# Optimization experiments

Measured on AMD Instinct MI355X. Metric: run time of the kernel, lower is better.

Reference implementation:

```python
import jax, jax.numpy as jnp
import numpy as np

R_MAX = 6.0
NUM_BASIS = 8
TANH_N = 6.0
RECYCLES = 3
N_NODES = 20000
N_EDGES = 640000
ATTR_DIM = 64
LATENT = 64
LN_EPS = 1e-5


def _layer_norm(x, g, b):
    m = x.mean(-1, keepdims=True)
    v = x.var(-1, keepdims=True)
    return (x - m) * jax.lax.rsqrt(v + LN_EPS) * g + b


def setup_inputs() -> dict:
    key = jax.random.key(0)
    ks = jax.random.split(key, 16)
    d1 = 2 * ATTR_DIM + NUM_BASIS  # 136, edge_feature_mlp input
    d2 = LATENT + ATTR_DIM         # 128, attn_mlp input
    d3 = 2 * LATENT                # 128, latent_update_mlp input
    s1 = 1.0 / np.sqrt(d1)
    s2 = 1.0 / np.sqrt(d2)
    s3 = 1.0 / np.sqrt(d3)
    sf = 1.0 / np.sqrt(NUM_BASIS)
    sg = 1.0 / np.sqrt(2 * LATENT)
    return {
        "edge_index": jax.random.randint(ks[0], (2, N_EDGES), 0, N_NODES, dtype=jnp.int64),
        "edge_length": jax.random.uniform(ks[1], (N_EDGES,), minval=0.5, maxval=R_MAX, dtype=jnp.float32),
        "node_attrs": jax.random.normal(ks[2], (N_NODES, ATTR_DIM), dtype=jnp.float32),
        "ln1_g": jnp.ones((d1,), jnp.float32), "ln1_b": jnp.zeros((d1,), jnp.float32),
        "W1": jax.random.normal(ks[3], (d1, LATENT), jnp.float32) * s1,
        "b1": jnp.zeros((LATENT,), jnp.float32),
        "ln2_g": jnp.ones((d2,), jnp.float32), "ln2_b": jnp.zeros((d2,), jnp.float32),
        "W2": jax.random.normal(ks[4], (d2, 1), jnp.float32) * s2,
        "b2": jnp.zeros((1,), jnp.float32),
        "ln3_g": jnp.ones((d3,), jnp.float32), "ln3_b": jnp.zeros((d3,), jnp.float32),
        "W3": jax.random.normal(ks[5], (d3, LATENT), jnp.float32) * s3,
        "b3": jnp.zeros((LATENT,), jnp.float32),
        "film_W1": jax.random.normal(ks[6], (NUM_BASIS, 4 * LATENT), jnp.float32) * sf,  # swiglu: 2*(2*latent)
        "film_W2": jax.random.normal(ks[7], (2 * LATENT, LATENT), jnp.float32) * sg,
        "resnet_p": jnp.zeros((1,), jnp.float32),
    }


def reference(edge_index, edge_length, node_attrs,
              ln1_g, ln1_b, W1, b1,
              ln2_g, ln2_b, W2, b2,
              ln3_g, ln3_b, W3, b3,
              film_W1, film_W2, resnet_p):
    ec = edge_index[0]
    en = edge_index[1]
    num_nodes = node_attrs.shape[0]
    num_edges = edge_index.shape[1]

    # Bessel radial basis * tanh cutoff
    n = jnp.arange(1, NUM_BASIS + 1, dtype=jnp.float32)
    r = edge_length[:, None]
    bessel = jnp.sqrt(2.0 / R_MAX) * jnp.sin(n * jnp.pi * r / R_MAX) / r  # [E, B]
    cutoff = jnp.tanh(1.0 - (edge_length / R_MAX) ** TANH_N) ** 3          # [E]
    rbf = bessel * cutoff[:, None]                                         # [E, B]

    a_c = node_attrs[ec]  # [E, A] gathered center attrs
    a_n = node_attrs[en]  # [E, A] gathered neighbor attrs

    latents = jnp.zeros((num_edges, LATENT), dtype=jnp.float32)
    for _ in range(RECYCLES):  # num_layers=1, recycles=3 -> 3 block applications
        edge_in = jnp.concatenate([a_c, a_n, rbf], axis=-1)            # [E, 136]
        ef = _layer_norm(edge_in, ln1_g, ln1_b) @ W1 + b1              # [E, L]
        attn_in = jnp.concatenate([ef, a_c], axis=-1)                  # [E, 128]
        scores = (_layer_norm(attn_in, ln2_g, ln2_b) @ W2 + b2)[:, 0]  # [E]
        attn = jax.nn.softmax(scores, axis=0)                          # global edge softmax
        pooled = jax.ops.segment_sum(attn[:, None] * ef, ec, num_segments=num_nodes)  # [N, L]
        upd_in = jnp.concatenate([ef, pooled[ec]], axis=-1)            # [E, 2L]
        upd = _layer_norm(upd_in, ln3_g, ln3_b) @ W3 + b3              # [E, L]
        # FiLM gate from rbf: swiglu hidden then sigmoid output, no bias
        h = rbf @ film_W1                                              # [E, 4L]
        a, g = jnp.split(h, 2, axis=-1)
        gate = jax.nn.sigmoid((jax.nn.silu(a) * g) @ film_W2)          # [E, L]
        upd = upd * gate
        uc = jax.nn.sigmoid(resnet_p)                                  # [1]
        c_old = jax.lax.rsqrt(uc * uc + 1.0)
        latents = c_old * latents + (uc * c_old) * upd
    return latents
```

## Files before the change

kernel.cpp:

```cpp
#include <hip/hip_runtime.h>
#include <math.h>

#define KNOTS 1024
#define LNE 1e-5f
#define R0F 0.5f
#define RMAXF 6.0f
#define PAD 96

__device__ __forceinline__ float hermite_(float v0, float m0, float v1, float m1, float t){
  float A = v1 - v0;
  return v0 + t*(m0 + t*((3.f*A - 2.f*m0 - m1) + t*(m0 + m1 - 2.f*A)));
}

__device__ __forceinline__ float wsum64(float v){
#pragma unroll
  for(int m=32;m>=1;m>>=1) v += __shfl_xor(v, m, 64);
  return v;
}

__global__ __launch_bounds__(256) void k_zero(int* cnt, float* sumExp, int N){
  int i = blockIdx.x*256 + threadIdx.x;
  if(i < N) cnt[i] = 0;
  if(i == 0) sumExp[0] = 0.f;
}

__global__ __launch_bounds__(256) void k_weights(
    const float* ln1_g, const float* ln1_b, const float* W1, const float* b1,
    const float* ln2_g, const float* ln2_b, const float* W2, const float* b2,
    const float* ln3_g, const float* ln3_b, const float* W3, const float* b3,
    const float* resnet_p,
    float* W1gA, float* W1gB, float* W1gBot, float* W3gTop, float* W3gBot,
    float* colsum1, float* c1, float* colsum3, float* c3, float* W2g,
    float* cs1w3, float* c1w3, float* BW3, float* misc){
  int tid = threadIdx.x;
  for(int idx=tid; idx<4096; idx+=256){
    int k = idx>>6;
    W1gA[idx]   = ln1_g[k]*W1[idx];
    W1gB[idx]   = ln1_g[64+k]*W1[4096+idx];
    W3gTop[idx] = ln3_g[k]*W3[idx];
    W3gBot[idx] = ln3_g[64+k]*W3[4096+idx];
  }
  for(int idx=tid; idx<512; idx+=256) W1gBot[idx] = ln1_g[128+(idx>>6)]*W1[8192+idx];
  if(tid<128) W2g[tid] = ln2_g[tid]*W2[tid];
  if(tid<64){
    float cs=0.f, cc=0.f;
    for(int k=0;k<136;k++){ float wv = W1[k*64+tid]; cs += ln1_g[k]*wv; cc += ln1_b[k]*wv; }
    colsum1[tid] = cs; c1[tid] = cc + b1[tid];
    float cs3=0.f, cc3=0.f;
    for(int k=0;k<128;k++){ float wv = W3[k*64+tid]; cs3 += ln3_g[k]*wv; cc3 += ln3_b[k]*wv; }
    colsum3[tid] = cs3; c3[tid] = cc3 + b3[tid];
  }
  if(tid==0){
    float cs2=0.f, cc2=0.f;
    for(int k=0;k<128;k++){ cs2 += ln2_g[k]*W2[k]; cc2 += ln2_b[k]*W2[k]; }
    misc[0]=cs2; misc[1]=cc2 + b2[0];
    float p = resnet_p[0];
    float uc = 1.f/(1.f+expf(-p));
    float co = rsqrtf(uc*uc+1.f);
    misc[2] = uc*co*(1.f + co + co*co);
  }
  __syncthreads();
  if(tid<64){
    float a=0.f, b=0.f;
    for(int k=0;k<64;k++){ float wv = W3gTop[k*64+tid]; a += colsum1[k]*wv; b += c1[k]*wv; }
    cs1w3[tid]=a; c1w3[tid]=b;
  }
  for(int idx=tid; idx<512; idx+=256){
    int kk = idx>>6, j = idx&63;
    float a=0.f;
    for(int k=0;k<64;k++) a += W1gBot[kk*64+k]*W3gTop[k*64+j];
    BW3[idx]=a;
  }
  if(tid==0){
    float a=0.f,b=0.f;
    for(int k=0;k<64;k++){ a += colsum1[k]*W2g[k]; b += c1[k]*W2g[k]; }
    misc[3]=a; misc[4]=b;
    float a5=0.f, a6=0.f;
    for(int k=0;k<64;k++){ a5 += colsum1[k]; a6 += c1[k]; }
    misc[5]=a5; misc[6]=a6;
  }
  if(tid<8){
    float a=0.f;
    for(int k=0;k<64;k++) a += W1gBot[tid*64+k]*W2g[k];
    misc[8+tid]=a;
  }
}

__device__ __forceinline__ void eval_all(
    float r, const float* W1gBot, const float* BW3, const float* bw2,
    const float* F1, const float* F2, float* uL, int lane,
    float& T1, float& T13, float& T12, float& gate, float& sr, float& sq){
  float rbf[8];
  float inv_r = 1.f/r;
  float x = r*(1.f/6.f);
  float x2 = x*x;
  float x6 = x2*x2*x2;
  float th = tanhf(1.f - x6);
  float cut = th*th*th;
  float pref = 0.57735026919f*inv_r*cut;
  sr=0.f; sq=0.f;
#pragma unroll
  for(int n=0;n<8;n++){
    float b = pref*sinf((float)(n+1)*0.52359877559f*r);
    rbf[n]=b; sr+=b; sq+=b*b;
  }
  float t1=0.f,t3=0.f,t2=0.f;
#pragma unroll
  for(int k=0;k<8;k++){
    t1 += rbf[k]*W1gBot[k*64+lane];
    t3 += rbf[k]*BW3[k*64+lane];
    t2 += rbf[k]*bw2[k];
  }
  T1=t1; T13=t3; T12=t2;
  float a0=0.f,a1=0.f,g0=0.f,g1=0.f;
#pragma unroll
  for(int k=0;k<8;k++){
    const float* row = F1 + k*256;
    float rb = rbf[k];
    a0 += rb*row[lane];      a1 += rb*row[64+lane];
    g0 += rb*row[128+lane];  g1 += rb*row[192+lane];
  }
  uL[lane]    = (a0/(1.f+expf(-a0)))*g0;
  uL[64+lane] = (a1/(1.f+expf(-a1)))*g1;
  float accv = 0.f;
  for(int i2=0;i2<128;i2++) accv += uL[i2]*F2[i2*64+lane];
  gate = 1.f/(1.f+expf(-accv));
}

__global__ __launch_bounds__(256) void k_tables(
    const float* W1gBot, const float* BW3, const float* misc,
    const float* F1, const float* F2,
    float* tabT1, float* tab2, float* tabS){
  __shared__ __align__(16) float u[4][128];
  int lane = threadIdx.x&63, w = threadIdx.x>>6;
  int knot = blockIdx.x*4 + w;
  if(knot > KNOTS) return;
  const float H = (RMAXF-R0F)/KNOTS;
  float r = R0F + knot*H;
  const float dh = 1e-3f;
  const float* bw2 = misc+8;
  float T1c,T13c,T12c,Gc,SRc,SQc, T1p,T13p,T12p,Gp,SRp,SQp, T1m,T13m,T12m,Gm,SRm,SQm;
  eval_all(r,    W1gBot,BW3,bw2,F1,F2,u[w],lane, T1c,T13c,T12c,Gc,SRc,SQc);
  eval_all(r+dh, W1gBot,BW3,bw2,F1,F2,u[w],lane, T1p,T13p,T12p,Gp,SRp,SQp);
  eval_all(r-dh, W1gBot,BW3,bw2,F1,F2,u[w],lane, T1m,T13m,T12m,Gm,SRm,SQm);
  float sc = H/(2.f*dh);
  float sT1c = wsum64(T1c), sT1p = wsum64(T1p), sT1m = wsum64(T1m);
  ((float2*)tabT1)[knot*64+lane] = make_float2(T1c, (T1p-T1m)*sc);
  ((float4*)tab2)[knot*64+lane]  = make_float4(T13c,(T13p-T13m)*sc, Gc,(Gp-Gm)*sc);
  if(lane==0){
    float* d = tabS + knot*8;
    d[0]=SRc; d[1]=(SRp-SRm)*sc; d[2]=SQc; d[3]=(SQp-SQm)*sc;
    d[4]=T12c; d[5]=(T12p-T12m)*sc; d[6]=sT1c; d[7]=(sT1p-sT1m)*sc;
  }
}

__global__ __launch_bounds__(256) void k_node(
    const float* attrs, const float* W1gA, const float* W1gB, const float* W3gTop, const float* W2g,
    float* P, float* Q, float* QW3, float* PW3R,
    float4* packC, float4* packN, float* sumP, int N){
  __shared__ __align__(16) float sb[4][192];
  int v = (blockIdx.x*256+threadIdx.x)>>6;
  int lane = threadIdx.x&63, w = (threadIdx.x>>6)&3;
  if(v>=N) return;
  const float* av = attrs + (size_t)v*64;
  float al = av[lane];
  sb[w][lane] = al;
  float s = wsum64(al), sqv = wsum64(al*al), t = wsum64(al*W2g[64+lane]);
  float p=0.f, q=0.f;
  const float4* avv = (const float4*)(&sb[w][0]);
#pragma unroll
  for(int kk=0;kk<16;kk++){
    float4 x = avv[kk];
    const float* wa = W1gA + kk*256 + lane;
    const float* wb = W1gB + kk*256 + lane;
    p += x.x*wa[0] + x.y*wa[64] + x.z*wa[128] + x.w*wa[192];
    q += x.x*wb[0] + x.y*wb[64] + x.z*wb[128] + x.w*wb[192];
  }
  P[v*64+lane]=p; Q[v*64+lane]=q;
  float sp = wsum64(p), sq2 = wsum64(q);
  float pw2 = wsum64(p*W2g[lane]), qw2 = wsum64(q*W2g[lane]);
  sb[w][64+lane]=p; sb[w][128+lane]=q;
  float ap=0.f, aq=0.f;
  const float4* pv = (const float4*)(&sb[w][64]);
  const float4* qv = (const float4*)(&sb[w][128]);
#pragma unroll
  for(int kk=0;kk<16;kk++){
    float4 xp = pv[kk], xq = qv[kk];
    const float* wc = W3gTop + kk*256 + lane;
    ap += xp.x*wc[0] + xp.y*wc[64] + xp.z*wc[128] + xp.w*wc[192];
    aq += xq.x*wc[0] + xq.y*wc[64] + xq.z*wc[128] + xq.w*wc[192];
  }
  PW3R[v*128 + 2*lane] = ap;
  QW3[v*64+lane] = aq;
  if(lane==0){
    packC[v] = make_float4(s, sqv, t, pw2);
    packN[v] = make_float4(s, sqv, sq2, qw2);
    sumP[v] = sp;
  }
}

__global__ __launch_bounds__(256) void k_bin(const int* ei, const float* elen,
                                             int* cnt, float4* binRec, int N, int E){
  int e = blockIdx.x*256+threadIdx.x;
  if(e<E){
    int c = ei[e]; c = min(max(c,0),N-1);
    int nb = ei[E+e]; nb = min(max(nb,0),N-1);
    float r = elen[e];
    int pos = atomicAdd(&cnt[c],1);
    if(pos < PAD)
      binRec[c*PAD+pos] = make_float4(__int_as_float(nb), r, __int_as_float(e), 0.f);
  }
}

__global__ __launch_bounds__(256) void k_pool(
    const float4* binRec, const int* cnt,
    const float* P, const float* Q, const float* sumP,
    const float4* packC, const float4* packN,
    const float* colsum1, const float* c1, const float* misc,
    const float* tabT1, const float* tabS,
    float* pooled, float4* aux, float* sumExp, int N){
  __shared__ __align__(16) float accLds[4][64];
  __shared__ float accELds[4];
  int v = blockIdx.x;
  int w = threadIdx.x>>6, lane = threadIdx.x&63;
  int deg = min(cnt[v], PAD);
  int quarter = (deg+3)>>2;
  int st = w*quarter, ed = min(deg, st+quarter);
  float colg1 = colsum1[lane], c1l = c1[lane];
  float cs2 = misc[0], c2v = misc[1], csw2 = misc[3], cw2 = misc[4];
  float sumCol = misc[5], sumC1 = misc[6];
  const float invH = (float)KNOTS/(RMAXF-R0F);
  float4 cp = packC[v];
  float Pl = P[v*64+lane];
  float sPv = sumP[v];
  int base = v*PAD;
  float acc = 0.f, accE = 0.f;
  if(st < ed){
    int i1 = min(st+1, ed-1);
    float4 rA = binRec[base+st], rB = binRec[base+i1];
    int na = __float_as_int(rA.x), nbb = __float_as_int(rB.x);
    float qA = Q[na*64+lane], qB = Q[nbb*64+lane];
    float4 npA = packN[na], npB = packN[nbb];
    for(int i=st; i<ed; i+=2){
      float4 recA=rA, recB=rB;
      float QlA=qA, QlB=qB;
      float4 nA=npA, nB=npB;
      bool hasB = (i+1) < ed;
      if(i+2 < ed){
        int p0 = i+2, p1 = min(i+3, ed-1);
        rA = binRec[base+p0]; rB = binRec[base+p1];
        int a2 = __float_as_int(rA.x), b2 = __float_as_int(rB.x);
        qA = Q[a2*64+lane]; qB = Q[b2*64+lane];
        npA = packN[a2]; npB = packN[b2];
      }
      float uuA = (recA.y - R0F)*invH;
      int tiA = (int)uuA; tiA = min(max(tiA,0),KNOTS-1);
      float ttA = uuA - (float)tiA;
      int tbA = tiA*64+lane;
      float2 a1A = ((const float2*)tabT1)[tbA], b1A = ((const float2*)tabT1)[tbA+64];
      const float* sA = tabS + tiA*8;
      float4 scaA = *(const float4*)sA, scbA = *(const float4*)(sA+8);
      float4 twaA = *(const float4*)(sA+4), twbA = *(const float4*)(sA+12);
      float uuB = (recB.y - R0F)*invH;
      int tiB = (int)uuB; tiB = min(max(tiB,0),KNOTS-1);
      float ttB = uuB - (float)tiB;
      int tbB = tiB*64+lane;
      float2 a1B = ((const float2*)tabT1)[tbB], b1B = ((const float2*)tabT1)[tbB+64];
      const float* sB = tabS + tiB*8;
      float4 scaB = *(const float4*)sB, scbB = *(const float4*)(sB+8);
      float4 twaB = *(const float4*)(sB+4), twbB = *(const float4*)(sB+12);

      float T1A  = hermite_(a1A.x,a1A.y,b1A.x,b1A.y,ttA);
      float srbA = hermite_(scaA.x,scaA.y,scbA.x,scbA.y,ttA);
      float sqbA = hermite_(scaA.z,scaA.w,scbA.z,scbA.w,ttA);
      float t1w2A= hermite_(twaA.x,twaA.y,twbA.x,twbA.y,ttA);
      float sT1A = hermite_(twaA.z,twaA.w,twbA.z,twbA.w,ttA);
      float T1B  = hermite_(a1B.x,a1B.y,b1B.x,b1B.y,ttB);
      float srbB = hermite_(scaB.x,scaB.y,scbB.x,scbB.y,ttB);
      float sqbB = hermite_(scaB.z,scaB.w,scbB.z,scbB.w,ttB);
      float t1w2B= hermite_(twaB.x,twaB.y,twbB.x,twbB.y,ttB);
      float sT1B = hermite_(twaB.z,twaB.w,twbB.z,twbB.w,ttB);

      float mA = (cp.x + nA.x + srbA)*(1.f/136.f);
      float varA = (cp.y + nA.y + sqbA)*(1.f/136.f) - mA*mA;
      float rsA = rsqrtf(varA + LNE);
      float efA = rsA*(Pl + QlA + T1A - mA*colg1) + c1l;
      float sumEfA = rsA*(sPv + nA.z + sT1A - mA*sumCol) + sumC1;
      float swA = rsA*(cp.w + nA.w + t1w2A - mA*csw2) + cw2;
      float mB = (cp.x + nB.x + srbB)*(1.f/136.f);
      float varB = (cp.y + nB.y + sqbB)*(1.f/136.f) - mB*mB;
      float rsB = rsqrtf(varB + LNE);
      float efB = rsB*(Pl + QlB + T1B - mB*colg1) + c1l;
      float sumEfB = rsB*(sPv + nB.z + sT1B - mB*sumCol) + sumC1;
      float swB = rsB*(cp.w + nB.w + t1w2B - mB*csw2) + cw2;

      float r1A = efA*efA, r1B = efB*efB;
#pragma unroll
      for(int msk=32; msk>=1; msk>>=1){
        r1A += __shfl_xor(r1A,msk,64);
        r1B += __shfl_xor(r1B,msk,64);
      }
      float m2A = (sumEfA + cp.x)*(1.f/128.f);
      float var2A = (r1A + cp.y)*(1.f/128.f) - m2A*m2A;
      float rs2A = rsqrtf(var2A + LNE);
      float scoreA = rs2A*(swA + cp.z - m2A*cs2) + c2v;
      float eevA = __expf(scoreA);
      acc += eevA*efA; accE += eevA;
      if(lane==0) aux[__float_as_int(recA.z)] = make_float4(r1A, rsA, mA, sumEfA);
      if(hasB){
        float m2B = (sumEfB + cp.x)*(1.f/128.f);
        float var2B = (r1B + cp.y)*(1.f/128.f) - m2B*m2B;
        float rs2B = rsqrtf(var2B + LNE);
        float scoreB = rs2B*(swB + cp.z - m2B*cs2) + c2v;
        float eevB = __expf(scoreB);
        acc += eevB*efB; accE += eevB;
        if(lane==0) aux[__float_as_int(recB.z)] = make_float4(r1B, rsB, mB, sumEfB);
      }
    }
  }
  accLds[w][lane] = acc;
  if(lane==0) accELds[w] = accE;
  __syncthreads();
  if(w==0){
    float a = accLds[0][lane]+accLds[1][lane]+accLds[2][lane]+accLds[3][lane];
    pooled[v*64+lane] = a;
    if(lane==0){
      float eT = accELds[0]+accELds[1]+accELds[2]+accELds[3];
      if(eT != 0.f) atomicAdd(sumExp, eT);
    }
  }
}

__global__ __launch_bounds__(256) void k_node2(
    const float* pooledRaw, const float* sumExp, const float* W3gBot, const float* sumP,
    float* PW3R, float4* packF, int N){
  __shared__ __align__(16) float sb[4][64];
  int v = (blockIdx.x*256+threadIdx.x)>>6;
  int lane = threadIdx.x&63, w = (threadIdx.x>>6)&3;
  if(v>=N) return;
  float inv = 1.f/sumExp[0];
  float pl = pooledRaw[v*64+lane]*inv;
  float s = wsum64(pl), sq = wsum64(pl*pl);
  sb[w][lane] = pl;
  float acc = 0.f;
  const float4* pv = (const float4*)(&sb[w][0]);
#pragma unroll
  for(int kk=0;kk<16;kk++){
    float4 x = pv[kk];
    const float* wc = W3gBot + kk*256 + lane;
    acc += x.x*wc[0] + x.y*wc[64] + x.z*wc[128] + x.w*wc[192];
  }
  PW3R[v*128 + 2*lane + 1] = acc;
  if(lane==0){ packF[v] = make_float4(s, sq, sumP[v], 0.f); }
}

#define FCHUNK 16
__global__ __launch_bounds__(256) void k_final(
    const int* ei, const float* elen, const float4* aux,
    const float* QW3, const float* PW3R, const float4* packF,
    const float* cs1w3, const float* c1w3, const float* colsum3, const float* c3,
    const float* misc, const float* tab2,
    float* out, int N, int E){
  int w = threadIdx.x>>6, lane = threadIdx.x&63;
  int st = (blockIdx.x*4 + w)*FCHUNK;
  if(st >= E) return;
  int ed = min(st+FCHUNK, E);
  float csw3 = cs1w3[lane], cw3 = c1w3[lane];
  float col3 = colsum3[lane], c3l = c3[lane];
  float SC = misc[2];
  const float invH = (float)KNOTS/(RMAXF-R0F);
  for(int i=st; i<ed; i+=2){
    int eA = i, eB = min(i+1, ed-1);
    int cA = ei[eA];   cA = min(max(cA,0),N-1);
    int nA = ei[E+eA]; nA = min(max(nA,0),N-1);
    int cB = ei[eB];   cB = min(max(cB,0),N-1);
    int nB = ei[E+eB]; nB = min(max(nB,0),N-1);
    float rrA = elen[eA], rrB = elen[eB];
    float4 xA = aux[eA], xB = aux[eB];
    float2 pwA = ((const float2*)PW3R)[cA*64+lane];
    float2 pwB = ((const float2*)PW3R)[cB*64+lane];
    float q3A = QW3[nA*64+lane];
    float q3B = QW3[nB*64+lane];
    float4 pfA = packF[cA], pfB = packF[cB];
    float uuA = (rrA - R0F)*invH;
    int tiA = (int)uuA; tiA = min(max(tiA,0),KNOTS-1);
    float ttA = uuA - (float)tiA;
    int tbA = tiA*64+lane;
    float uuB = (rrB - R0F)*invH;
    int tiB = (int)uuB; tiB = min(max(tiB,0),KNOTS-1);
    float ttB = uuB - (float)tiB;
    int tbB = tiB*64+lane;
    float4 t2aA = ((const float4*)tab2)[tbA], t2bA = ((const float4*)tab2)[tbA+64];
    float4 t2aB = ((const float4*)tab2)[tbB], t2bB = ((const float4*)tab2)[tbB+64];
    {
      float T13 = hermite_(t2aA.x,t2aA.y,t2bA.x,t2bA.y,ttA);
      float gate= hermite_(t2aA.z,t2aA.w,t2bA.z,t2bA.w,ttA);
      float r1 = xA.x, rs = xA.y, m = xA.z, sEf = xA.w;
      float efd = rs*(pwA.x + q3A + T13 - m*csw3) + cw3;
      float m3 = (sEf + pfA.x)*(1.f/128.f);
      float var3 = (r1 + pfA.y)*(1.f/128.f) - m3*m3;
      float rs3 = rsqrtf(var3 + LNE);
      float upd = rs3*(efd + pwA.y - m3*col3) + c3l;
      out[(size_t)eA*64 + lane] = SC*upd*gate;
    }
    {
      float T13 = hermite_(t2aB.x,t2aB.y,t2bB.x,t2bB.y,ttB);
      float gate= hermite_(t2aB.z,t2aB.w,t2bB.z,t2bB.w,ttB);
      float r1 = xB.x, rs = xB.y, m = xB.z, sEf = xB.w;
      float efd = rs*(pwB.x + q3B + T13 - m*csw3) + cw3;
      float m3 = (sEf + pfB.x)*(1.f/128.f);
      float var3 = (r1 + pfB.y)*(1.f/128.f) - m3*m3;
      float rs3 = rsqrtf(var3 + LNE);
      float upd = rs3*(efd + pwB.y - m3*col3) + c3l;
      out[(size_t)eB*64 + lane] = SC*upd*gate;
    }
  }
}

extern "C" void kernel_launch(void* const* d_in, const int* in_sizes, int n_in,
                              void* d_out, int out_size, void* d_ws, size_t ws_size,
                              hipStream_t stream){
  const int*   ei    = (const int*)  d_in[0];
  const float* elen  = (const float*)d_in[1];
  const float* attrs = (const float*)d_in[2];
  const float* ln1_g = (const float*)d_in[3];
  const float* ln1_b = (const float*)d_in[4];
  const float* W1    = (const float*)d_in[5];
  const float* b1    = (const float*)d_in[6];
  const float* ln2_g = (const float*)d_in[7];
  const float* ln2_b = (const float*)d_in[8];
  const float* W2    = (const float*)d_in[9];
  const float* b2    = (const float*)d_in[10];
  const float* ln3_g = (const float*)d_in[11];
  const float* ln3_b = (const float*)d_in[12];
  const float* W3    = (const float*)d_in[13];
  const float* b3    = (const float*)d_in[14];
  const float* F1    = (const float*)d_in[15];
  const float* F2    = (const float*)d_in[16];
  const float* resp  = (const float*)d_in[17];
  const int E = in_sizes[1];
  const int N = in_sizes[2]/64;
  float* ws = (float*)d_ws;
  size_t o = 0;
  auto A = [&](size_t n){ size_t rr = o; o += (n + 63) & ~(size_t)63; return rr; };
  float* P      = ws + A((size_t)N*64);
  float* Q      = ws + A((size_t)N*64);
  float* QW3    = ws + A((size_t)N*64);
  float* PW3R   = ws + A((size_t)N*128);
  float* pooled = ws + A((size_t)N*64);
  float* sumP   = ws + A(N);
  float4* packC = (float4*)(ws + A((size_t)N*4));
  float4* packN = (float4*)(ws + A((size_t)N*4));
  float4* packF = (float4*)(ws + A((size_t)N*4));
  float* W1gA   = ws + A(4096);
  float* W1gB   = ws + A(4096);
  float* W1gBot = ws + A(512);
  float* W3gTop = ws + A(4096);
  float* W3gBot = ws + A(4096);
  float* BW3    = ws + A(512);
  float* colsum1= ws + A(64);
  float* c1     = ws + A(64);
  float* cs1w3  = ws + A(64);
  float* c1w3   = ws + A(64);
  float* colsum3= ws + A(64);
  float* c3     = ws + A(64);
  float* W2g    = ws + A(128);
  float* misc   = ws + A(64);
  float* tabT1  = ws + A((size_t)(KNOTS+1)*128);
  float* tab2   = ws + A((size_t)(KNOTS+1)*256);
  float* tabS   = ws + A((size_t)(KNOTS+1)*8);
  float* sumExp = ws + A(64);
  int* cnt      = (int*)(ws + A((size_t)N));
  float4* binRec= (float4*)(ws + A((size_t)N*PAD*4));
  float4* aux   = (float4*)(ws + A((size_t)E*4));
  (void)ws_size; (void)out_size; (void)n_in;
  float* out = (float*)d_out;

  int nb4 = (N+3)/4;
  k_zero<<<(N+255)/256, 256, 0, stream>>>(cnt, sumExp, N);
  k_weights<<<1,256,0,stream>>>(ln1_g,ln1_b,W1,b1,ln2_g,ln2_b,W2,b2,ln3_g,ln3_b,W3,b3,resp,
      W1gA,W1gB,W1gBot,W3gTop,W3gBot,colsum1,c1,colsum3,c3,W2g,cs1w3,c1w3,BW3,misc);
  k_tables<<<(KNOTS+4)/4, 256, 0, stream>>>(W1gBot,BW3,misc,F1,F2,tabT1,tab2,tabS);
  k_node<<<nb4,256,0,stream>>>(attrs,W1gA,W1gB,W3gTop,W2g,P,Q,QW3,PW3R,packC,packN,sumP,N);
  k_bin<<<(E+255)/256,256,0,stream>>>(ei,elen,cnt,binRec,N,E);
  k_pool<<<N,256,0,stream>>>(binRec,cnt,P,Q,sumP,packC,packN,colsum1,c1,misc,tabT1,tabS,pooled,aux,sumExp,N);
  k_node2<<<nb4,256,0,stream>>>(pooled,sumExp,W3gBot,sumP,PW3R,packF,N);
  {
    int chunks = (E + FCHUNK - 1)/FCHUNK;
    int blocks = (chunks + 3)/4;
    k_final<<<blocks,256,0,stream>>>(ei,elen,aux,QW3,PW3R,packF,cs1w3,c1w3,colsum3,c3,misc,tab2,out,N,E);
  }
}
```

Measured before the change: 727.8 us.

## Precompute per-edge LN scalars algebraically and assign one wave per node in pool

The sum of squares of the edge feature vector is expanded algebraically into per-node moments, per-knot table moments and a single P·Q dot product, which removes the second per-edge reduction over ef. A lane-parallel prepass computes each edge's scalars into shared memory. The per-lane T1 table is replaced by an interpolated 8-wide RBF table, and the pooling kernel now assigns one wave per node instead of one 256-thread block, which drops the cross-wave LDS reduction. The trade-offs are more per-node reductions in k_node, a large shared-memory array that may limit occupancy, and possible precision loss from the expanded variance formula.

```diff
diff --git a/kernel.cpp b/kernel.cpp
--- a/kernel.cpp
+++ b/kernel.cpp
@@ -78,6 +78,9 @@
     float a5=0.f, a6=0.f;
     for(int k=0;k<64;k++){ a5 += colsum1[k]; a6 += c1[k]; }
     misc[5]=a5; misc[6]=a6;
+    float gg=0.f, gc=0.f, ccs=0.f;
+    for(int k=0;k<64;k++){ float g=colsum1[k], c=c1[k]; gg+=g*g; gc+=g*c; ccs+=c*c; }
+    misc[16]=gg; misc[17]=gc; misc[18]=ccs;
   }
   if(tid<8){
     float a=0.f;
@@ -88,7 +91,7 @@
 
 __device__ __forceinline__ void eval_all(
     float r, const float* W1gBot, const float* BW3, const float* bw2,
-    const float* F1, const float* F2, float* uL, int lane,
+    const float* F1, const float* F2, float* uL, int lane, float* rbfO,
     float& T1, float& T13, float& T12, float& gate, float& sr, float& sq){
   float rbf[8];
   float inv_r = 1.f/r;
@@ -102,7 +105,7 @@
 #pragma unroll
   for(int n=0;n<8;n++){
     float b = pref*sinf((float)(n+1)*0.52359877559f*r);
-    rbf[n]=b; sr+=b; sq+=b*b;
+    rbf[n]=b; rbfO[n]=b; sr+=b; sq+=b*b;
   }
   float t1=0.f,t3=0.f,t2=0.f;
 #pragma unroll
@@ -129,8 +132,8 @@
 
 __global__ __launch_bounds__(256) void k_tables(
     const float* W1gBot, const float* BW3, const float* misc,
-    const float* F1, const float* F2,
-    float* tabT1, float* tab2, float* tabS){
+    const float* F1, const float* F2, const float* colsum1, const float* c1,
+    float* tab2, float* tabS, float* tabRbf){
   __shared__ __align__(16) float u[4][128];
   int lane = threadIdx.x&63, w = threadIdx.x>>6;
   int knot = blockIdx.x*4 + w;
@@ -139,25 +142,35 @@
   float r = R0F + knot*H;
   const float dh = 1e-3f;
   const float* bw2 = misc+8;
+  float rbc[8], rbp[8], rbm[8];
   float T1c,T13c,T12c,Gc,SRc,SQc, T1p,T13p,T12p,Gp,SRp,SQp, T1m,T13m,T12m,Gm,SRm,SQm;
-  eval_all(r,    W1gBot,BW3,bw2,F1,F2,u[w],lane, T1c,T13c,T12c,Gc,SRc,SQc);
-  eval_all(r+dh, W1gBot,BW3,bw2,F1,F2,u[w],lane, T1p,T13p,T12p,Gp,SRp,SQp);
-  eval_all(r-dh, W1gBot,BW3,bw2,F1,F2,u[w],lane, T1m,T13m,T12m,Gm,SRm,SQm);
+  eval_all(r,    W1gBot,BW3,bw2,F1,F2,u[w],lane, rbc, T1c,T13c,T12c,Gc,SRc,SQc);
+  eval_all(r+dh, W1gBot,BW3,bw2,F1,F2,u[w],lane, rbp, T1p,T13p,T12p,Gp,SRp,SQp);
+  eval_all(r-dh, W1gBot,BW3,bw2,F1,F2,u[w],lane, rbm, T1m,T13m,T12m,Gm,SRm,SQm);
   float sc = H/(2.f*dh);
+  float cg = colsum1[lane], cl = c1[lane];
   float sT1c = wsum64(T1c), sT1p = wsum64(T1p), sT1m = wsum64(T1m);
-  ((float2*)tabT1)[knot*64+lane] = make_float2(T1c, (T1p-T1m)*sc);
-  ((float4*)tab2)[knot*64+lane]  = make_float4(T13c,(T13p-T13m)*sc, Gc,(Gp-Gm)*sc);
+  float T11c = wsum64(T1c*T1c), T11p = wsum64(T1p*T1p), T11m = wsum64(T1m*T1m);
+  float T1gc = wsum64(T1c*cg), T1gp = wsum64(T1p*cg), T1gm = wsum64(T1m*cg);
+  float T1cc = wsum64(T1c*cl), T1cp = wsum64(T1p*cl), T1cm = wsum64(T1m*cl);
+  ((float4*)tab2)[knot*64+lane] = make_float4(T13c,(T13p-T13m)*sc, Gc,(Gp-Gm)*sc);
   if(lane==0){
-    float* d = tabS + knot*8;
-    d[0]=SRc; d[1]=(SRp-SRm)*sc; d[2]=SQc; d[3]=(SQp-SQm)*sc;
+    float* d = tabS + knot*16;
+    d[0]=SRc;  d[1]=(SRp-SRm)*sc;   d[2]=SQc;  d[3]=(SQp-SQm)*sc;
     d[4]=T12c; d[5]=(T12p-T12m)*sc; d[6]=sT1c; d[7]=(sT1p-sT1m)*sc;
+    d[8]=T11c; d[9]=(T11p-T11m)*sc; d[10]=T1gc; d[11]=(T1gp-T1gm)*sc;
+    d[12]=T1cc; d[13]=(T1cp-T1cm)*sc; d[14]=0.f; d[15]=0.f;
+    float* rb = tabRbf + knot*16;
+#pragma unroll
+    for(int k=0;k<8;k++){ rb[2*k]=rbc[k]; rb[2*k+1]=(rbp[k]-rbm[k])*sc; }
   }
 }
 
 __global__ __launch_bounds__(256) void k_node(
-    const float* attrs, const float* W1gA, const float* W1gB, const float* W3gTop, const float* W2g,
+    const float* attrs, const float* W1gA, const float* W1gB, const float* W3gTop,
+    const float* W2g, const float* W1gBot, const float* colsum1, const float* c1,
     float* P, float* Q, float* QW3, float* PW3R,
-    float4* packC, float4* packN, float* sumP, int N){
+    float* nodeC, float* nodeN, int N){
   __shared__ __align__(16) float sb[4][192];
   int v = (blockIdx.x*256+threadIdx.x)>>6;
   int lane = threadIdx.x&63, w = (threadIdx.x>>6)&3;
@@ -179,6 +192,17 @@
   P[v*64+lane]=p; Q[v*64+lane]=q;
   float sp = wsum64(p), sq2 = wsum64(q);
   float pw2 = wsum64(p*W2g[lane]), qw2 = wsum64(q*W2g[lane]);
+  float cg = colsum1[lane], cl = c1[lane];
+  float SPP = wsum64(p*p), SQQ = wsum64(q*q);
+  float SPg = wsum64(p*cg), SQg = wsum64(q*cg);
+  float SPc = wsum64(p*cl), SQc = wsum64(q*cl);
+  float pbv[8], qbv[8];
+#pragma unroll
+  for(int k=0;k<8;k++){
+    float wv = W1gBot[k*64+lane];
+    pbv[k] = wsum64(p*wv);
+    qbv[k] = wsum64(q*wv);
+  }
   sb[w][64+lane]=p; sb[w][128+lane]=q;
   float ap=0.f, aq=0.f;
   const float4* pv = (const float4*)(&sb[w][64]);
@@ -193,9 +217,14 @@
   PW3R[v*128 + 2*lane] = ap;
   QW3[v*64+lane] = aq;
   if(lane==0){
-    packC[v] = make_float4(s, sqv, t, pw2);
-    packN[v] = make_float4(s, sqv, sq2, qw2);
-    sumP[v] = sp;
+    float* nc = nodeC + v*16;
+    nc[0]=s; nc[1]=sqv; nc[2]=t; nc[3]=pw2; nc[4]=SPP; nc[5]=SPg; nc[6]=SPc; nc[7]=sp;
+#pragma unroll
+    for(int k=0;k<8;k++) nc[8+k]=pbv[k];
+    float* nn = nodeN + v*16;
+    nn[0]=s; nn[1]=sqv; nn[2]=sq2; nn[3]=qw2; nn[4]=SQQ; nn[5]=SQg; nn[6]=SQc; nn[7]=0.f;
+#pragma unroll
+    for(int k=0;k<8;k++) nn[8+k]=qbv[k];
   }
 }
 
@@ -214,125 +243,145 @@
 
 __global__ __launch_bounds__(256) void k_pool(
     const float4* binRec, const int* cnt,
-    const float* P, const float* Q, const float* sumP,
-    const float4* packC, const float4* packN,
+    const float* P, const float* Q,
+    const float* nodeC, const float* nodeN, const float* W1gBot,
     const float* colsum1, const float* c1, const float* misc,
-    const float* tabT1, const float* tabS,
+    const float* tabS, const float* tabRbf,
     float* pooled, float4* aux, float* sumExp, int N){
-  __shared__ __align__(16) float accLds[4][64];
-  __shared__ float accELds[4];
-  int v = blockIdx.x;
+  __shared__ float scal[4][PAD][17];
   int w = threadIdx.x>>6, lane = threadIdx.x&63;
-  int deg = min(cnt[v], PAD);
-  int quarter = (deg+3)>>2;
-  int st = w*quarter, ed = min(deg, st+quarter);
-  float colg1 = colsum1[lane], c1l = c1[lane];
-  float cs2 = misc[0], c2v = misc[1], csw2 = misc[3], cw2 = misc[4];
-  float sumCol = misc[5], sumC1 = misc[6];
+  int v = blockIdx.x*4 + w;
+  int vv = min(v, N-1);
+  int deg = (v<N) ? min(cnt[vv], PAD) : 0;
   const float invH = (float)KNOTS/(RMAXF-R0F);
-  float4 cp = packC[v];
-  float Pl = P[v*64+lane];
-  float sPv = sumP[v];
-  int base = v*PAD;
+  int base = vv*PAD;
+  {
+    float cc0=nodeC[vv*16+0], cc1=nodeC[vv*16+1], cc3=nodeC[vv*16+3];
+    float cc4=nodeC[vv*16+4], cc5=nodeC[vv*16+5], cc6=nodeC[vv*16+6], cc7=nodeC[vv*16+7];
+    float pb[8];
+#pragma unroll
+    for(int k=0;k<8;k++) pb[k]=nodeC[vv*16+8+k];
+    float csw2=misc[3], cw2=misc[4], sumCol=misc[5], sumC1=misc[6];
+    float Sgg=misc[16], Sgc1=misc[17], Sc1c1=misc[18];
+    for(int slot=lane; slot<deg; slot+=64){
+      float4 rec = binRec[base+slot];
+      int nb = __float_as_int(rec.x);
+      float r = rec.y;
+      float uu = (r-R0F)*invH;
+      int ti = (int)uu; ti = min(max(ti,0),KNOTS-1);
+      float tt = uu-(float)ti;
+      const float4* sA4 = (const float4*)(tabS + ti*16);
+      const float4* sB4 = (const float4*)(tabS + (ti+1)*16);
+      float4 sA0=sA4[0], sA1=sA4[1], sA2=sA4[2], sA3=sA4[3];
+      float4 sB0=sB4[0], sB1=sB4[1], sB2=sB4[2], sB3=sB4[3];
+      const float4* rA4 = (const float4*)(tabRbf + ti*16);
+      const float4* rB4 = (const float4*)(tabRbf + (ti+1)*16);
+      float rbf[8];
+      {
+        float4 a0=rA4[0], a1=rA4[1], a2=rA4[2], a3=rA4[3];
+        float4 b0=rB4[0], b1=rB4[1], b2=rB4[2], b3=rB4[3];
+        rbf[0]=hermite_(a0.x,a0.y,b0.x,b0.y,tt); rbf[1]=hermite_(a0.z,a0.w,b0.z,b0.w,tt);
+        rbf[2]=hermite_(a1.x,a1.y,b1.x,b1.y,tt); rbf[3]=hermite_(a1.z,a1.w,b1.z,b1.w,tt);
+        rbf[4]=hermite_(a2.x,a2.y,b2.x,b2.y,tt); rbf[5]=hermite_(a2.z,a2.w,b2.z,b2.w,tt);
+        rbf[6]=hermite_(a3.x,a3.y,b3.x,b3.y,tt); rbf[7]=hermite_(a3.z,a3.w,b3.z,b3.w,tt);
+      }
+      float srb = hermite_(sA0.x,sA0.y,sB0.x,sB0.y,tt);
+      float sqb = hermite_(sA0.z,sA0.w,sB0.z,sB0.w,tt);
+      float t1w2= hermite_(sA1.x,sA1.y,sB1.x,sB1.y,tt);
+      float sT1 = hermite_(sA1.z,sA1.w,sB1.z,sB1.w,tt);
+      float T11 = hermite_(sA2.x,sA2.y,sB2.x,sB2.y,tt);
+      float T1g = hermite_(sA2.z,sA2.w,sB2.z,sB2.w,tt);
+      float T1c1= hermite_(sA3.x,sA3.y,sB3.x,sB3.y,tt);
+      const float4* nn4 = (const float4*)(nodeN + (size_t)nb*16);
+      float4 nn0=nn4[0], nn1=nn4[1], nn2=nn4[2], nn3=nn4[3];
+      float PT1 = rbf[0]*pb[0]+rbf[1]*pb[1]+rbf[2]*pb[2]+rbf[3]*pb[3]
+                + rbf[4]*pb[4]+rbf[5]*pb[5]+rbf[6]*pb[6]+rbf[7]*pb[7];
+      float QT1 = rbf[0]*nn2.x+rbf[1]*nn2.y+rbf[2]*nn2.z+rbf[3]*nn2.w
+                + rbf[4]*nn3.x+rbf[5]*nn3.y+rbf[6]*nn3.z+rbf[7]*nn3.w;
+      float m = (cc0 + nn0.x + srb)*(1.f/136.f);
+      float var = (cc1 + nn0.y + sqb)*(1.f/136.f) - m*m;
+      float rs = rsqrtf(var + LNE);
+      float sumEf = rs*(cc7 + nn0.z + sT1 - m*sumCol) + sumC1;
+      float sw = rs*(cc3 + nn0.w + t1w2 - m*csw2) + cw2;
+      float SS0 = rs*rs*(cc4 + nn1.x + T11 + 2.f*(PT1+QT1)
+                          - 2.f*m*(cc5 + nn1.y + T1g) + m*m*Sgg)
+                + 2.f*rs*(cc6 + nn1.z + T1c1 - m*Sgc1) + Sc1c1;
+      float* L = &scal[w][slot][0];
+      L[0]=rs; L[1]=m; L[2]=sumEf; L[3]=sw; L[4]=SS0; L[5]=2.f*rs*rs;
+#pragma unroll
+      for(int k=0;k<8;k++) L[6+k]=rbf[k];
+    }
+  }
+  __syncthreads();
   float acc = 0.f, accE = 0.f;
-  if(st < ed){
-    int i1 = min(st+1, ed-1);
-    float4 rA = binRec[base+st], rB = binRec[base+i1];
-    int na = __float_as_int(rA.x), nbb = __float_as_int(rB.x);
-    float qA = Q[na*64+lane], qB = Q[nbb*64+lane];
-    float4 npA = packN[na], npB = packN[nbb];
-    for(int i=st; i<ed; i+=2){
-      float4 recA=rA, recB=rB;
-      float QlA=qA, QlB=qB;
-      float4 nA=npA, nB=npB;
-      bool hasB = (i+1) < ed;
-      if(i+2 < ed){
-        int p0 = i+2, p1 = min(i+3, ed-1);
+  if(v < N && deg > 0){
+    float Pl = P[vv*64+lane];
+    float colg1 = colsum1[lane], c1l = c1[lane];
+    float w1b[8];
+#pragma unroll
+    for(int k=0;k<8;k++) w1b[k] = W1gBot[k*64+lane];
+    float cc0=nodeC[vv*16+0], cc1=nodeC[vv*16+1], cc2=nodeC[vv*16+2];
+    float cs2=misc[0], c2v=misc[1];
+    const float inv128 = 1.f/128.f;
+    int i1 = min(1, deg-1);
+    float4 rA = binRec[base], rB = binRec[base+i1];
+    float qA = Q[__float_as_int(rA.x)*64+lane];
+    float qB = Q[__float_as_int(rB.x)*64+lane];
+    for(int i=0; i<deg; i+=2){
+      float4 recA = rA, recB = rB;
+      float QlA = qA, QlB = qB;
+      bool hasB = (i+1) < deg;
+      int iB = min(i+1, deg-1);
+      if(i+2 < deg){
+        int p0 = i+2, p1 = min(i+3, deg-1);
         rA = binRec[base+p0]; rB = binRec[base+p1];
-        int a2 = __float_as_int(rA.x), b2 = __float_as_int(rB.x);
-        qA = Q[a2*64+lane]; qB = Q[b2*64+lane];
-        npA = packN[a2]; npB = packN[b2];
+        qA = Q[__float_as_int(rA.x)*64+lane];
+        qB = Q[__float_as_int(rB.x)*64+lane];
       }
-      float uuA = (recA.y - R0F)*invH;
-      int tiA = (int)uuA; tiA = min(max(tiA,0),KNOTS-1);
-      float ttA = uuA - (float)tiA;
-      int tbA = tiA*64+lane;
-      float2 a1A = ((const float2*)tabT1)[tbA], b1A = ((const float2*)tabT1)[tbA+64];
-      const float* sA = tabS + tiA*8;
-      float4 scaA = *(const float4*)sA, scbA = *(const float4*)(sA+8);
-      float4 twaA = *(const float4*)(sA+4), twbA = *(const float4*)(sA+12);
-      float uuB = (recB.y - R0F)*invH;
-      int tiB = (int)uuB; tiB = min(max(tiB,0),KNOTS-1);
-      float ttB = uuB - (float)tiB;
-      int tbB = tiB*64+lane;
-      float2 a1B = ((const float2*)tabT1)[tbB], b1B = ((const float2*)tabT1)[tbB+64];
-      const float* sB = tabS + tiB*8;
-      float4 scaB = *(const float4*)sB, scbB = *(const float4*)(sB+8);
-      float4 twaB = *(const float4*)(sB+4), twbB = *(const float4*)(sB+12);
-
-      float T1A  = hermite_(a1A.x,a1A.y,b1A.x,b1A.y,ttA);
-      float srbA = hermite_(scaA.x,scaA.y,scbA.x,scbA.y,ttA);
-      float sqbA = hermite_(scaA.z,scaA.w,scbA.z,scbA.w,ttA);
-      float t1w2A= hermite_(twaA.x,twaA.y,twbA.x,twbA.y,ttA);
-      float sT1A = hermite_(twaA.z,twaA.w,twbA.z,twbA.w,ttA);
-      float T1B  = hermite_(a1B.x,a1B.y,b1B.x,b1B.y,ttB);
-      float srbB = hermite_(scaB.x,scaB.y,scbB.x,scbB.y,ttB);
-      float sqbB = hermite_(scaB.z,scaB.w,scbB.z,scbB.w,ttB);
-      float t1w2B= hermite_(twaB.x,twaB.y,twbB.x,twbB.y,ttB);
-      float sT1B = hermite_(twaB.z,twaB.w,twbB.z,twbB.w,ttB);
-
-      float mA = (cp.x + nA.x + srbA)*(1.f/136.f);
-      float varA = (cp.y + nA.y + sqbA)*(1.f/136.f) - mA*mA;
-      float rsA = rsqrtf(varA + LNE);
+      const float* LA = &scal[w][i][0];
+      const float* LB = &scal[w][iB][0];
+      float rsA=LA[0], mA=LA[1], seA=LA[2], swA=LA[3], S0A=LA[4], cdA=LA[5];
+      float rsB=LB[0], mB=LB[1], seB=LB[2], swB=LB[3], S0B=LB[4], cdB=LB[5];
+      float T1A = LA[6]*w1b[0]+LA[7]*w1b[1]+LA[8]*w1b[2]+LA[9]*w1b[3]
+                + LA[10]*w1b[4]+LA[11]*w1b[5]+LA[12]*w1b[6]+LA[13]*w1b[7];
+      float T1B = LB[6]*w1b[0]+LB[7]*w1b[1]+LB[8]*w1b[2]+LB[9]*w1b[3]
+                + LB[10]*w1b[4]+LB[11]*w1b[5]+LB[12]*w1b[6]+LB[13]*w1b[7];
       float efA = rsA*(Pl + QlA + T1A - mA*colg1) + c1l;
-      float sumEfA = rsA*(sPv + nA.z + sT1A - mA*sumCol) + sumC1;
-      float swA = rsA*(cp.w + nA.w + t1w2A - mA*csw2) + cw2;
-      float mB = (cp.x + nB.x + srbB)*(1.f/136.f);
-      float varB = (cp.y + nB.y + sqbB)*(1.f/136.f) - mB*mB;
-      float rsB = rsqrtf(varB + LNE);
       float efB = rsB*(Pl + QlB + T1B - mB*colg1) + c1l;
-      float sumEfB = rsB*(sPv + nB.z + sT1B - mB*sumCol) + sumC1;
-      float swB = rsB*(cp.w + nB.w + t1w2B - mB*csw2) + cw2;
-
-      float r1A = efA*efA, r1B = efB*efB;
+      float dA = Pl*QlA, dB = Pl*QlB;
 #pragma unroll
       for(int msk=32; msk>=1; msk>>=1){
-        r1A += __shfl_xor(r1A,msk,64);
-        r1B += __shfl_xor(r1B,msk,64);
+        dA += __shfl_xor(dA,msk,64);
+        dB += __shfl_xor(dB,msk,64);
       }
-      float m2A = (sumEfA + cp.x)*(1.f/128.f);
-      float var2A = (r1A + cp.y)*(1.f/128.f) - m2A*m2A;
+      float r1A = S0A + cdA*dA;
+      float m2A = (seA + cc0)*inv128;
+      float var2A = (r1A + cc1)*inv128 - m2A*m2A;
       float rs2A = rsqrtf(var2A + LNE);
-      float scoreA = rs2A*(swA + cp.z - m2A*cs2) + c2v;
+      float scoreA = rs2A*(swA + cc2 - m2A*cs2) + c2v;
       float eevA = __expf(scoreA);
       acc += eevA*efA; accE += eevA;
-      if(lane==0) aux[__float_as_int(recA.z)] = make_float4(r1A, rsA, mA, sumEfA);
+      if(lane==0) aux[__float_as_int(recA.z)] = make_float4(r1A, rsA, mA, seA);
       if(hasB){
-        float m2B = (sumEfB + cp.x)*(1.f/128.f);
-        float var2B = (r1B + cp.y)*(1.f/128.f) - m2B*m2B;
+        float r1B = S0B + cdB*dB;
+        float m2B = (seB + cc0)*inv128;
+        float var2B = (r1B + cc1)*inv128 - m2B*m2B;
         float rs2B = rsqrtf(var2B + LNE);
-        float scoreB = rs2B*(swB + cp.z - m2B*cs2) + c2v;
+        float scoreB = rs2B*(swB + cc2 - m2B*cs2) + c2v;
         float eevB = __expf(scoreB);
         acc += eevB*efB; accE += eevB;
-        if(lane==0) aux[__float_as_int(recB.z)] = make_float4(r1B, rsB, mB, sumEfB);
+        if(lane==0) aux[__float_as_int(recB.z)] = make_float4(r1B, rsB, mB, seB);
       }
     }
   }
-  accLds[w][lane] = acc;
-  if(lane==0) accELds[w] = accE;
-  __syncthreads();
-  if(w==0){
-    float a = accLds[0][lane]+accLds[1][lane]+accLds[2][lane]+accLds[3][lane];
-    pooled[v*64+lane] = a;
-    if(lane==0){
-      float eT = accELds[0]+accELds[1]+accELds[2]+accELds[3];
-      if(eT != 0.f) atomicAdd(sumExp, eT);
-    }
+  if(v < N){
+    pooled[vv*64+lane] = acc;
+    if(lane==0 && accE != 0.f) atomicAdd(sumExp, accE);
   }
 }
 
 __global__ __launch_bounds__(256) void k_node2(
-    const float* pooledRaw, const float* sumExp, const float* W3gBot, const float* sumP,
+    const float* pooledRaw, const float* sumExp, const float* W3gBot, const float* nodeC,
     float* PW3R, float4* packF, int N){
   __shared__ __align__(16) float sb[4][64];
   int v = (blockIdx.x*256+threadIdx.x)>>6;
@@ -351,7 +400,7 @@
     acc += x.x*wc[0] + x.y*wc[64] + x.z*wc[128] + x.w*wc[192];
   }
   PW3R[v*128 + 2*lane + 1] = acc;
-  if(lane==0){ packF[v] = make_float4(s, sq, sumP[v], 0.f); }
+  if(lane==0){ packF[v] = make_float4(s, sq, nodeC[v*16+7], 0.f); }
 }
 
 #define FCHUNK 16
@@ -448,9 +497,8 @@
   float* QW3    = ws + A((size_t)N*64);
   float* PW3R   = ws + A((size_t)N*128);
   float* pooled = ws + A((size_t)N*64);
-  float* sumP   = ws + A(N);
-  float4* packC = (float4*)(ws + A((size_t)N*4));
-  float4* packN = (float4*)(ws + A((size_t)N*4));
+  float* nodeC  = ws + A((size_t)N*16);
+  float* nodeN  = ws + A((size_t)N*16);
   float4* packF = (float4*)(ws + A((size_t)N*4));
   float* W1gA   = ws + A(4096);
   float* W1gB   = ws + A(4096);
@@ -466,9 +514,9 @@
   float* c3     = ws + A(64);
   float* W2g    = ws + A(128);
   float* misc   = ws + A(64);
-  float* tabT1  = ws + A((size_t)(KNOTS+1)*128);
   float* tab2   = ws + A((size_t)(KNOTS+1)*256);
-  float* tabS   = ws + A((size_t)(KNOTS+1)*8);
+  float* tabS   = ws + A((size_t)(KNOTS+1)*16);
+  float* tabRbf = ws + A((size_t)(KNOTS+1)*16);
   float* sumExp = ws + A(64);
   int* cnt      = (int*)(ws + A((size_t)N));
   float4* binRec= (float4*)(ws + A((size_t)N*PAD*4));
@@ -480,11 +528,11 @@
   k_zero<<<(N+255)/256, 256, 0, stream>>>(cnt, sumExp, N);
   k_weights<<<1,256,0,stream>>>(ln1_g,ln1_b,W1,b1,ln2_g,ln2_b,W2,b2,ln3_g,ln3_b,W3,b3,resp,
       W1gA,W1gB,W1gBot,W3gTop,W3gBot,colsum1,c1,colsum3,c3,W2g,cs1w3,c1w3,BW3,misc);
-  k_tables<<<(KNOTS+4)/4, 256, 0, stream>>>(W1gBot,BW3,misc,F1,F2,tabT1,tab2,tabS);
-  k_node<<<nb4,256,0,stream>>>(attrs,W1gA,W1gB,W3gTop,W2g,P,Q,QW3,PW3R,packC,packN,sumP,N);
+  k_tables<<<(KNOTS+4)/4, 256, 0, stream>>>(W1gBot,BW3,misc,F1,F2,colsum1,c1,tab2,tabS,tabRbf);
+  k_node<<<nb4,256,0,stream>>>(attrs,W1gA,W1gB,W3gTop,W2g,W1gBot,colsum1,c1,P,Q,QW3,PW3R,nodeC,nodeN,N);
   k_bin<<<(E+255)/256,256,0,stream>>>(ei,elen,cnt,binRec,N,E);
-  k_pool<<<N,256,0,stream>>>(binRec,cnt,P,Q,sumP,packC,packN,colsum1,c1,misc,tabT1,tabS,pooled,aux,sumExp,N);
-  k_node2<<<nb4,256,0,stream>>>(pooled,sumExp,W3gBot,sumP,PW3R,packF,N);
+  k_pool<<<nb4,256,0,stream>>>(binRec,cnt,P,Q,nodeC,nodeN,W1gBot,colsum1,c1,misc,tabS,tabRbf,pooled,aux,sumExp,N);
+  k_node2<<<nb4,256,0,stream>>>(pooled,sumExp,W3gBot,nodeC,PW3R,packF,N);
   {
     int chunks = (E + FCHUNK - 1)/FCHUNK;
     int blocks = (chunks + 3)/4;
```

Result: slower. 748.3 us (+2.8%).
